# Kernel optimization log

Hardware: AMD Instinct MI355X
Metric: run time of the kernel (lower is better)

## Reference

```python
import jax, jax.numpy as jnp
import numpy as np

SHIFT_MIN, SHIFT_MAX = -14.0, 0.0  # deepshift range for weight_bits=5: (-(2**4-2), 0)


def shift_quant(w):
    """Quantize weights to signed powers of two (bit-shift weights), STE form."""
    sign = jnp.sign(w)
    shift = jnp.clip(jnp.round(jnp.log2(jnp.abs(w) + 1e-12)), SHIFT_MIN, SHIFT_MAX)
    q = sign * jnp.exp2(shift)
    return w + jax.lax.stop_gradient(q - w)


def moe_fc(t, wg, w0, b0, w1, b1):
    """Top-1 routing over 2 experts: expert0 dense Linear, expert1 shift-quantized Linear.
    t: [T, C]; weights torch-layout [out, in]. With top_k=1 the softmaxed top-k gate is 1.0,
    so combine is a hard select of the chosen expert's output."""
    logits = t @ wg                      # [T, 2]
    pick0 = (jnp.argmax(logits, axis=-1) == 0)[:, None]
    y0 = t @ w0.T + b0                   # dense expert
    y1 = t @ shift_quant(w1).T + b1      # shift expert
    return jnp.where(pick0, y0, y1)


def setup_inputs() -> dict:
    key = jax.random.key(0)
    ks = jax.random.split(key, 10)
    B, N, C, Dh = 16, 1024, 512, 2048
    s = 0.02
    return {
        "x": jax.random.normal(ks[0], (B, N, C), jnp.float32),
        "H": 32,
        "W": 32,
        "wg1": jax.random.normal(ks[1], (C, 2), jnp.float32) * s,
        "fc1_w0": jax.random.normal(ks[2], (Dh, C), jnp.float32) * s,
        "fc1_b0": jnp.zeros((Dh,), jnp.float32),
        "fc1_w1": jax.random.normal(ks[3], (Dh, C), jnp.float32) * s,
        "fc1_b1": jnp.zeros((Dh,), jnp.float32),
        "dw_w": jax.random.normal(ks[4], (Dh, 1, 3, 3), jnp.float32) * np.sqrt(2.0 / 9.0),
        "dw_b": jnp.zeros((Dh,), jnp.float32),
        "wg2": jax.random.normal(ks[5], (Dh, 2), jnp.float32) * s,
        "fc2_w0": jax.random.normal(ks[6], (C, Dh), jnp.float32) * s,
        "fc2_b0": jnp.zeros((C,), jnp.float32),
        "fc2_w1": jax.random.normal(ks[7], (C, Dh), jnp.float32) * s,
        "fc2_b1": jnp.zeros((C,), jnp.float32),
    }


def reference(x, H, W, wg1, fc1_w0, fc1_b0, fc1_w1, fc1_b1, dw_w, dw_b,
              wg2, fc2_w0, fc2_b0, fc2_w1, fc2_b1):
    B, N, C = x.shape
    Dh = fc1_w0.shape[0]
    # fc1 MoE
    h = moe_fc(x.reshape(-1, C), wg1, fc1_w0, fc1_b0, fc1_w1, fc1_b1)  # [B*N, Dh]
    # DWConv 3x3 depthwise, NCHW
    h = h.reshape(B, N, Dh).transpose(0, 2, 1).reshape(B, Dh, H, W)
    h = jax.lax.conv_general_dilated(
        h, dw_w, window_strides=(1, 1), padding="SAME",
        dimension_numbers=("NCHW", "OIHW", "NCHW"), feature_group_count=Dh)
    h = h + dw_b[None, :, None, None]
    h = h.reshape(B, Dh, N).transpose(0, 2, 1)  # [B, N, Dh]
    # GELU (exact, as nn.GELU default); dropout p=0 -> identity
    h = jax.nn.gelu(h, approximate=False)
    # fc2 MoE
    y = moe_fc(h.reshape(-1, Dh), wg2, fc2_w0, fc2_b0, fc2_w1, fc2_b1)
    return y.reshape(B, N, -1)
```

## Files before the change

### kernel.cpp

```cpp
#include <hip/hip_runtime.h>
#include <hip/hip_bf16.h>


#define TOKS  16384
#define CIN   512
#define DHID  2048

typedef __attribute__((ext_vector_type(8))) __bf16 bf16x8;
typedef __attribute__((ext_vector_type(4))) float  f32x4;
typedef __attribute__((ext_vector_type(4))) float  float4v;
typedef __attribute__((ext_vector_type(4))) unsigned short ushort4v;
typedef __attribute__((ext_vector_type(8))) unsigned short ushort8;

__device__ __forceinline__ unsigned short f2bf(float f) {
  union { float f; unsigned int u; } a; a.f = f;
  unsigned int u = a.u;
  unsigned int r = u + 0x7FFFu + ((u >> 16) & 1u);
  return (unsigned short)(r >> 16);
}
__device__ __forceinline__ float bf2f(unsigned short h) {
  union { unsigned int u; float f; } a; a.u = ((unsigned int)h) << 16;
  return a.f;
}

__device__ __forceinline__ float squant(float w) {
  if (w == 0.0f) return 0.0f;
  float aw = fabsf(w) + 1e-12f;
  union { float f; unsigned u; } a; a.f = aw;
  int e = (int)((a.u >> 23) & 0xFFu) - 127;
  unsigned frac = a.u & 0x7FFFFFu;
  int shift = e + (frac >= 0x3504F4u ? 1 : 0);
  shift = min(max(shift, -14), 0);
  union { unsigned u; float f; } q; q.u = (unsigned)(shift + 127) << 23;
  return (w > 0.0f) ? q.f : -q.f;
}

#define GLDS16(gp, lp) __builtin_amdgcn_global_load_lds(                      \
    (const __attribute__((address_space(1))) void*)(gp),                      \
    (__attribute__((address_space(3))) void*)(lp), 16, 0, 0)

#define SBAR()  { __builtin_amdgcn_s_barrier(); __builtin_amdgcn_sched_barrier(0); }
#define VMCNT(n) asm volatile("s_waitcnt vmcnt(" #n ")" ::: "memory")

__global__ void k_prep(const float* __restrict__ w0, const float* __restrict__ w1,
                       const float* __restrict__ w20, const float* __restrict__ w21,
                       unsigned short* __restrict__ w0hi, unsigned short* __restrict__ w0lo,
                       unsigned short* __restrict__ w1q, unsigned short* __restrict__ w20b,
                       unsigned short* __restrict__ w21b) {
  int i = blockIdx.x * 256 + threadIdx.x;
  if (i >= DHID * CIN) return;
  float v = w0[i];
  unsigned short h = f2bf(v);
  w0hi[i] = h;
  w0lo[i] = f2bf(v - bf2f(h));
  w1q[i]  = f2bf(squant(w1[i]));
  w20b[i] = f2bf(w20[i]);
  w21b[i] = f2bf(squant(w21[i]));
}

__global__ void k_prepg(const float* __restrict__ x, const float* __restrict__ wg1,
                        unsigned short* __restrict__ xhi, unsigned short* __restrict__ xlo,
                        unsigned char* __restrict__ pick1) {
  __shared__ float wg[1024];
  const int t = threadIdx.x;
  #pragma unroll
  for (int i = 0; i < 4; ++i) wg[t + i * 256] = wg1[t + i * 256];
  __syncthreads();
  const int tok = blockIdx.x * 4 + (t >> 6);
  const int l = t & 63;
  const float* xr = x + (size_t)tok * CIN + l * 8;
  float4v v0 = *(const float4v*)xr;
  float4v v1 = *(const float4v*)(xr + 4);
  float s0 = 0.f, s1 = 0.f;
  ushort8 hv, lv;
  #pragma unroll
  for (int j = 0; j < 8; ++j) {
    float v = (j < 4) ? v0[j] : v1[j - 4];
    unsigned short h = f2bf(v);
    hv[j] = h;
    lv[j] = f2bf(v - bf2f(h));
    int c = l * 8 + j;
    s0 += v * wg[c * 2];
    s1 += v * wg[c * 2 + 1];
  }
  *(ushort8*)&xhi[(size_t)tok * CIN + l * 8] = hv;
  *(ushort8*)&xlo[(size_t)tok * CIN + l * 8] = lv;
  for (int m = 32; m; m >>= 1) { s0 += __shfl_xor(s0, m); s1 += __shfl_xor(s1, m); }
  if (l == 0) pick1[tok] = (s0 >= s1) ? 0 : 1;
}

__global__ void k_scan(const unsigned char* __restrict__ pick, int* __restrict__ perm,
                       int* __restrict__ n0buf) {
  __shared__ int wpre[17];
  const int t = threadIdx.x;
  const int lane = t & 63, w = t >> 6;
  unsigned char loc[16]; int c0 = 0;
  #pragma unroll
  for (int i = 0; i < 16; ++i) { loc[i] = pick[t * 16 + i]; c0 += (loc[i] == 0); }
  int s = c0;
  #pragma unroll
  for (int off = 1; off < 64; off <<= 1) {
    int v = __shfl_up(s, off);
    if (lane >= off) s += v;
  }
  if (lane == 63) wpre[w + 1] = s;
  if (t == 0) wpre[0] = 0;
  __syncthreads();
  if (t == 0) {
    for (int j = 1; j <= 16; ++j) wpre[j] += wpre[j - 1];
    n0buf[0] = wpre[16];
  }
  __syncthreads();
  int total0 = wpre[16];
  int pre0 = wpre[w] + s - c0;
  int pre1 = t * 16 - pre0;
  int p0 = pre0, p1 = total0 + pre1;
  #pragma unroll
  for (int i = 0; i < 16; ++i) {
    int tok = t * 16 + i;
    if (loc[i] == 0) perm[p0++] = tok; else perm[p1++] = tok;
  }
}

__launch_bounds__(256, 2)
__global__ void k_fc1_e0(const unsigned short* __restrict__ xhi,
                         const unsigned short* __restrict__ xlo,
                         const unsigned short* __restrict__ w0hi,
                         const unsigned short* __restrict__ w0lo,
                         const float* __restrict__ b0,
                         const int* __restrict__ perm, const int* __restrict__ n0buf,
                         float* __restrict__ h32) {
  __shared__ unsigned short sm[24576];
  const int n0 = n0buf[0];
  const int t = threadIdx.x, wv = t >> 6, ln = t & 63;
  const int lr = ln & 15, lg = ln >> 4;
  const int g = blockIdx.x, q = g >> 3;
  const int tok0 = ((g & 7) + ((q >> 4) << 3)) * 128;
  const int nbase = (q & 15) * 128;
  if (tok0 >= n0) return;
  const int wm = (wv >> 1) * 64, wn = (wv & 1) * 64;

  int rowoff[4];
  #pragma unroll
  for (int mt = 0; mt < 4; ++mt)
    rowoff[mt] = perm[tok0 + wm + (mt << 4) + lr] * CIN + (lg << 3);

  const int swsrc = (((ln & 3) ^ ((ln >> 3) & 3)) << 3);
  const int swrd  = ((lg ^ ((lr >> 1) & 3)) << 3);

  f32x4 acc[4][4];
  #pragma unroll
  for (int i = 0; i < 4; ++i)
    #pragma unroll
    for (int j = 0; j < 4; ++j) acc[i][j] = f32x4{0.f, 0.f, 0.f, 0.f};

  auto STAGEB = [&](int kt, int db) {
    const int k0 = kt * 32;
    #pragma unroll
    for (int s = 0; s < 2; ++s) {
      const int rowblk = s * 4 + wv;
      size_t gb = (size_t)(nbase + (rowblk << 4) + (ln >> 2)) * CIN + k0 + swsrc;
      GLDS16(w0hi + gb, &sm[db * 8192 + (rowblk << 9)]);
      GLDS16(w0lo + gb, &sm[db * 8192 + 4096 + (rowblk << 9)]);
    }
  };
  auto LOADA = [&](bf16x8 (&ah)[4], bf16x8 (&al)[4], int kt) {
    const int k0 = kt * 32;
    #pragma unroll
    for (int mt = 0; mt < 4; ++mt) {
      ah[mt] = *(const bf16x8*)&xhi[rowoff[mt] + k0];
      al[mt] = *(const bf16x8*)&xlo[rowoff[mt] + k0];
    }
  };
  auto COMPUTE = [&](const bf16x8 (&ah)[4], const bf16x8 (&al)[4], int db) {
    __builtin_amdgcn_s_setprio(1);
    #pragma unroll
    for (int nt = 0; nt < 4; ++nt) {
      int bb = db * 8192 + (wn + (nt << 4) + lr) * 32 + swrd;
      bf16x8 bh = *(const bf16x8*)&sm[bb];
      bf16x8 bl = *(const bf16x8*)&sm[bb + 4096];
      #pragma unroll
      for (int mt = 0; mt < 4; ++mt) {
        acc[mt][nt] = __builtin_amdgcn_mfma_f32_16x16x32_bf16(ah[mt], bh, acc[mt][nt], 0, 0, 0);
        acc[mt][nt] = __builtin_amdgcn_mfma_f32_16x16x32_bf16(al[mt], bh, acc[mt][nt], 0, 0, 0);
        acc[mt][nt] = __builtin_amdgcn_mfma_f32_16x16x32_bf16(ah[mt], bl, acc[mt][nt], 0, 0, 0);
      }
    }
    __builtin_amdgcn_s_setprio(0);
  };

  bf16x8 Ah0[4], Al0[4], Ah1[4], Al1[4];
  LOADA(Ah0, Al0, 0);
  STAGEB(0, 0);
  STAGEB(1, 1);
  for (int kt = 0; kt < 14; kt += 2) {
    SBAR();
    LOADA(Ah1, Al1, kt + 1);
    STAGEB(kt + 2, (kt + 2) % 3);
    VMCNT(16);
    SBAR();
    COMPUTE(Ah0, Al0, kt % 3);
    SBAR();
    LOADA(Ah0, Al0, kt + 2);
    STAGEB(kt + 3, (kt + 3) % 3);
    VMCNT(16);
    SBAR();
    COMPUTE(Ah1, Al1, (kt + 1) % 3);
  }
  SBAR();
  LOADA(Ah1, Al1, 15);
  VMCNT(12);
  SBAR();
  COMPUTE(Ah0, Al0, 2);
  SBAR();
  VMCNT(0);
  SBAR();
  COMPUTE(Ah1, Al1, 0);

  __syncthreads();
  float* smf = (float*)sm;
  float bi[4];
  #pragma unroll
  for (int nt = 0; nt < 4; ++nt) bi[nt] = b0[nbase + wn + (nt << 4) + lr];
  #pragma unroll
  for (int mt = 0; mt < 4; ++mt) {
    #pragma unroll
    for (int nt = 0; nt < 4; ++nt) {
      f32x4 v = acc[mt][nt];
      #pragma unroll
      for (int rr = 0; rr < 4; ++rr)
        smf[wv * 1088 + ((lg << 2) + rr) * 68 + (nt << 4) + lr] = v[rr] + bi[nt];
    }
    #pragma unroll
    for (int p = 0; p < 4; ++p) {
      int row = (p << 2) + (ln >> 4);
      int pos = tok0 + wm + (mt << 4) + row;
      if (pos < n0) {
        f32x4 vv = *(const f32x4*)&smf[wv * 1088 + row * 68 + ((ln & 15) << 2)];
        *(f32x4*)&h32[(size_t)perm[pos] * DHID + nbase + wn + ((ln & 15) << 2)] = vv;
      }
    }
  }
}

__launch_bounds__(256, 2)
__global__ void k_fc1_e1(const unsigned short* __restrict__ xhi,
                         const unsigned short* __restrict__ xlo,
                         const unsigned short* __restrict__ w1q,
                         const float* __restrict__ b1,
                         const int* __restrict__ perm, const int* __restrict__ n0buf,
                         float* __restrict__ h32) {
  __shared__ unsigned short sm[12288];
  const int n0 = n0buf[0];
  const int t = threadIdx.x, wv = t >> 6, ln = t & 63;
  const int lr = ln & 15, lg = ln >> 4;
  const int g = blockIdx.x, q = g >> 3;
  const int tok0 = ((g & 7) + ((q >> 4) << 3)) * 128;
  const int nbase = (q & 15) * 128;
  if (tok0 + 128 <= n0) return;
  const int wm = (wv >> 1) * 64, wn = (wv & 1) * 64;

  int rowoff[4];
  #pragma unroll
  for (int mt = 0; mt < 4; ++mt)
    rowoff[mt] = perm[tok0 + wm + (mt << 4) + lr] * CIN + (lg << 3);

  const int swsrc = (((ln & 3) ^ ((ln >> 3) & 3)) << 3);
  const int swrd  = ((lg ^ ((lr >> 1) & 3)) << 3);

  f32x4 acc[4][4];
  #pragma unroll
  for (int i = 0; i < 4; ++i)
    #pragma unroll
    for (int j = 0; j < 4; ++j) acc[i][j] = f32x4{0.f, 0.f, 0.f, 0.f};

  auto STAGEB = [&](int kt, int db) {
    const int k0 = kt * 32;
    #pragma unroll
    for (int s = 0; s < 2; ++s) {
      const int rowblk = s * 4 + wv;
      size_t gb = (size_t)(nbase + (rowblk << 4) + (ln >> 2)) * CIN + k0 + swsrc;
      GLDS16(w1q + gb, &sm[db * 4096 + (rowblk << 9)]);
    }
  };
  auto LOADA = [&](bf16x8 (&ah)[4], bf16x8 (&al)[4], int kt) {
    const int k0 = kt * 32;
    #pragma unroll
    for (int mt = 0; mt < 4; ++mt) {
      ah[mt] = *(const bf16x8*)&xhi[rowoff[mt] + k0];
      al[mt] = *(const bf16x8*)&xlo[rowoff[mt] + k0];
    }
  };
  auto COMPUTE = [&](const bf16x8 (&ah)[4], const bf16x8 (&al)[4], int db) {
    __builtin_amdgcn_s_setprio(1);
    #pragma unroll
    for (int nt = 0; nt < 4; ++nt) {
      bf16x8 bq = *(const bf16x8*)&sm[db * 4096 + (wn + (nt << 4) + lr) * 32 + swrd];
      #pragma unroll
      for (int mt = 0; mt < 4; ++mt) {
        acc[mt][nt] = __builtin_amdgcn_mfma_f32_16x16x32_bf16(ah[mt], bq, acc[mt][nt], 0, 0, 0);
        acc[mt][nt] = __builtin_amdgcn_mfma_f32_16x16x32_bf16(al[mt], bq, acc[mt][nt], 0, 0, 0);
      }
    }
    __builtin_amdgcn_s_setprio(0);
  };

  bf16x8 Ah0[4], Al0[4], Ah1[4], Al1[4];
  LOADA(Ah0, Al0, 0);
  STAGEB(0, 0);
  STAGEB(1, 1);
  for (int kt = 0; kt < 14; kt += 2) {
    SBAR();
    LOADA(Ah1, Al1, kt + 1);
    STAGEB(kt + 2, (kt + 2) % 3);
    VMCNT(12);
    SBAR();
    COMPUTE(Ah0, Al0, kt % 3);
    SBAR();
    LOADA(Ah0, Al0, kt + 2);
    STAGEB(kt + 3, (kt + 3) % 3);
    VMCNT(12);
    SBAR();
    COMPUTE(Ah1, Al1, (kt + 1) % 3);
  }
  SBAR();
  LOADA(Ah1, Al1, 15);
  VMCNT(10);
  SBAR();
  COMPUTE(Ah0, Al0, 2);
  SBAR();
  VMCNT(0);
  SBAR();
  COMPUTE(Ah1, Al1, 0);

  __syncthreads();
  float* smf = (float*)sm;
  float bi[4];
  #pragma unroll
  for (int nt = 0; nt < 4; ++nt) bi[nt] = b1[nbase + wn + (nt << 4) + lr];
  #pragma unroll
  for (int mt = 0; mt < 4; ++mt) {
    #pragma unroll
    for (int nt = 0; nt < 4; ++nt) {
      f32x4 v = acc[mt][nt];
      #pragma unroll
      for (int rr = 0; rr < 4; ++rr)
        smf[wv * 1088 + ((lg << 2) + rr) * 68 + (nt << 4) + lr] = v[rr] + bi[nt];
    }
    #pragma unroll
    for (int p = 0; p < 4; ++p) {
      int row = (p << 2) + (ln >> 4);
      int pos = tok0 + wm + (mt << 4) + row;
      if (pos >= n0) {
        f32x4 vv = *(const f32x4*)&smf[wv * 1088 + row * 68 + ((ln & 15) << 2)];
        *(f32x4*)&h32[(size_t)perm[pos] * DHID + nbase + wn + ((ln & 15) << 2)] = vv;
      }
    }
  }
}

__launch_bounds__(256)
__global__ void k_conv(const float* __restrict__ h32, const float* __restrict__ dww,
                       const float* __restrict__ dwb, const float* __restrict__ wg2,
                       unsigned short* __restrict__ hb, float* __restrict__ part) {
  __shared__ float4v tile[10][32][8];
  const int dc = blockIdx.x;
  const int ys = blockIdx.y;
  const int b  = blockIdx.z;
  const int t = threadIdx.x;
  const int d0 = dc * 32, y0 = ys * 8;
  const int dl4 = t & 7, xq = t >> 3;

  #pragma unroll
  for (int ry = 0; ry < 10; ++ry) {
    int y = y0 - 1 + ry;
    float4v v = {0.f, 0.f, 0.f, 0.f};
    if (y >= 0 && y < 32)
      v = *(const float4v*)&h32[(size_t)(b * 1024 + y * 32 + xq) * DHID + d0 + dl4 * 4];
    tile[ry][xq][dl4] = v;
  }
  __syncthreads();

  const int d = d0 + dl4 * 4;
  float4v kk[9];
  #pragma unroll
  for (int i = 0; i < 9; ++i) {
    kk[i][0] = dww[(d + 0) * 9 + i]; kk[i][1] = dww[(d + 1) * 9 + i];
    kk[i][2] = dww[(d + 2) * 9 + i]; kk[i][3] = dww[(d + 3) * 9 + i];
  }
  const float4v bias = *(const float4v*)&dwb[d];
  float4v g0v, g1v;
  #pragma unroll
  for (int j = 0; j < 4; ++j) { g0v[j] = wg2[(d + j) * 2]; g1v[j] = wg2[(d + j) * 2 + 1]; }

  #pragma unroll
  for (int yy = 0; yy < 8; ++yy) {
    float4v s = bias;
    #pragma unroll
    for (int dy = 0; dy < 3; ++dy)
      #pragma unroll
      for (int dx = 0; dx < 3; ++dx) {
        int xs = xq + dx - 1;
        if (xs >= 0 && xs < 32) {
          float4v v = tile[yy + dy][xs][dl4];
          float4v k = kk[dy * 3 + dx];
          s[0] += v[0] * k[0]; s[1] += v[1] * k[1];
          s[2] += v[2] * k[2]; s[3] += v[3] * k[3];
        }
      }
    float4v gg;
    #pragma unroll
    for (int j = 0; j < 4; ++j)
      gg[j] = 0.5f * s[j] * (1.0f + erff(s[j] * 0.70710678118654752f));
    int tok = b * 1024 + (y0 + yy) * 32 + xq;
    ushort4v hv;
    #pragma unroll
    for (int j = 0; j < 4; ++j) hv[j] = f2bf(gg[j]);
    *(ushort4v*)&hb[(size_t)tok * DHID + d] = hv;
    float p0 = gg[0] * g0v[0] + gg[1] * g0v[1] + gg[2] * g0v[2] + gg[3] * g0v[3];
    float p1 = gg[0] * g1v[0] + gg[1] * g1v[1] + gg[2] * g1v[2] + gg[3] * g1v[3];
    p0 += __shfl_xor(p0, 1); p0 += __shfl_xor(p0, 2); p0 += __shfl_xor(p0, 4);
    p1 += __shfl_xor(p1, 1); p1 += __shfl_xor(p1, 2); p1 += __shfl_xor(p1, 4);
    if (dl4 == 0) {
      part[(size_t)tok * 128 + dc] = p0;
      part[(size_t)tok * 128 + 64 + dc] = p1;
    }
  }
}

__global__ void k_gate2(const float* __restrict__ part, unsigned char* __restrict__ pick2) {
  int tok = blockIdx.x * 4 + (threadIdx.x >> 6);
  int l = threadIdx.x & 63;
  const float* pr = part + (size_t)tok * 128;
  float s0 = pr[l], s1 = pr[64 + l];
  for (int m = 32; m; m >>= 1) { s0 += __shfl_xor(s0, m); s1 += __shfl_xor(s1, m); }
  if (l == 0) pick2[tok] = (s0 >= s1) ? 0 : 1;
}

template <int EXPERT>
__launch_bounds__(256, 2)
__global__ void k_fc2_e(const unsigned short* __restrict__ hb,
                        const unsigned short* __restrict__ wb,
                        const float* __restrict__ bias_v,
                        const int* __restrict__ perm, const int* __restrict__ n0buf,
                        float* __restrict__ out) {
  __shared__ unsigned short sm[24576];
  const int n0 = n0buf[0];
  const int t = threadIdx.x, wv = t >> 6, ln = t & 63;
  const int lr = ln & 15, lg = ln >> 4;
  const int g = blockIdx.x, q = g >> 3;
  const int tok0 = ((g & 7) + ((q >> 2) << 3)) * 128;
  const int nbase = (q & 3) * 128;
  if (EXPERT == 0) { if (tok0 >= n0) return; }
  else             { if (tok0 + 128 <= n0) return; }
  const int wm = (wv >> 1) * 64, wn = (wv & 1) * 64;

  int rowoff[4];
  #pragma unroll
  for (int mt = 0; mt < 4; ++mt)
    rowoff[mt] = perm[tok0 + wm + (mt << 4) + lr] * DHID + (lg << 3);

  const int swsrc = (((ln & 3) ^ ((ln >> 3) & 3)) << 3);
  const int swrd  = ((lg ^ ((lr >> 1) & 3)) << 3);

  f32x4 acc[4][4];
  #pragma unroll
  for (int i = 0; i < 4; ++i)
    #pragma unroll
    for (int j = 0; j < 4; ++j) acc[i][j] = f32x4{0.f, 0.f, 0.f, 0.f};

  auto STAGEB = [&](int kt, int db) {
    #pragma unroll
    for (int ks = 0; ks < 2; ++ks) {
      const int k0 = kt * 64 + ks * 32;
      #pragma unroll
      for (int s = 0; s < 2; ++s) {
        const int rowblk = s * 4 + wv;
        size_t gb = (size_t)(nbase + (rowblk << 4) + (ln >> 2)) * DHID + k0 + swsrc;
        GLDS16(wb + gb, &sm[db * 8192 + ks * 4096 + (rowblk << 9)]);
      }
    }
  };
  auto LOADA = [&](bf16x8 (&a)[8], int kt) {
    #pragma unroll
    for (int ks = 0; ks < 2; ++ks) {
      const int k0 = kt * 64 + ks * 32;
      #pragma unroll
      for (int mt = 0; mt < 4; ++mt)
        a[ks * 4 + mt] = *(const bf16x8*)&hb[rowoff[mt] + k0];
    }
  };
  auto COMPUTE = [&](const bf16x8 (&a)[8], int db) {
    __builtin_amdgcn_s_setprio(1);
    #pragma unroll
    for (int ks = 0; ks < 2; ++ks) {
      #pragma unroll
      for (int nt = 0; nt < 4; ++nt) {
        bf16x8 bf = *(const bf16x8*)&sm[db * 8192 + ks * 4096 + (wn + (nt << 4) + lr) * 32 + swrd];
        #pragma unroll
        for (int mt = 0; mt < 4; ++mt)
          acc[mt][nt] = __builtin_amdgcn_mfma_f32_16x16x32_bf16(a[ks * 4 + mt], bf, acc[mt][nt], 0, 0, 0);
      }
    }
    __builtin_amdgcn_s_setprio(0);
  };

  bf16x8 A0[8], A1[8];
  LOADA(A0, 0);
  STAGEB(0, 0);
  STAGEB(1, 1);
  for (int kt = 0; kt < 30; kt += 2) {
    SBAR();
    LOADA(A1, kt + 1);
    STAGEB(kt + 2, (kt + 2) % 3);
    VMCNT(16);
    SBAR();
    COMPUTE(A0, kt % 3);
    SBAR();
    LOADA(A0, kt + 2);
    STAGEB(kt + 3, (kt + 3) % 3);
    VMCNT(16);
    SBAR();
    COMPUTE(A1, (kt + 1) % 3);
  }
  SBAR();
  LOADA(A1, 31);
  VMCNT(12);
  SBAR();
  COMPUTE(A0, 0);
  SBAR();
  VMCNT(0);
  SBAR();
  COMPUTE(A1, 1);

  __syncthreads();
  float* smf = (float*)sm;
  float bi[4];
  #pragma unroll
  for (int nt = 0; nt < 4; ++nt) bi[nt] = bias_v[nbase + wn + (nt << 4) + lr];
  #pragma unroll
  for (int mt = 0; mt < 4; ++mt) {
    #pragma unroll
    for (int nt = 0; nt < 4; ++nt) {
      f32x4 v = acc[mt][nt];
      #pragma unroll
      for (int rr = 0; rr < 4; ++rr)
        smf[wv * 1088 + ((lg << 2) + rr) * 68 + (nt << 4) + lr] = v[rr] + bi[nt];
    }
    #pragma unroll
    for (int p = 0; p < 4; ++p) {
      int row = (p << 2) + (ln >> 4);
      int pos = tok0 + wm + (mt << 4) + row;
      bool store = (EXPERT == 0) ? (pos < n0) : (pos >= n0);
      if (store) {
        f32x4 vv = *(const f32x4*)&smf[wv * 1088 + row * 68 + ((ln & 15) << 2)];
        *(f32x4*)&out[(size_t)perm[pos] * CIN + nbase + wn + ((ln & 15) << 2)] = vv;
      }
    }
  }
}

extern "C" void kernel_launch(void* const* d_in, const int* in_sizes, int n_in,
                              void* d_out, int out_size, void* d_ws, size_t ws_size,
                              hipStream_t stream) {
  (void)in_sizes; (void)n_in; (void)out_size; (void)ws_size;
  const float* x   = (const float*)d_in[0];
  const float* wg1 = (const float*)d_in[3];
  const float* w0  = (const float*)d_in[4];
  const float* b0  = (const float*)d_in[5];
  const float* w1  = (const float*)d_in[6];
  const float* b1  = (const float*)d_in[7];
  const float* dww = (const float*)d_in[8];
  const float* dwb = (const float*)d_in[9];
  const float* wg2 = (const float*)d_in[10];
  const float* w20 = (const float*)d_in[11];
  const float* b20 = (const float*)d_in[12];
  const float* w21 = (const float*)d_in[13];
  const float* b21 = (const float*)d_in[14];
  float* out = (float*)d_out;

  char* ws = (char*)d_ws;
  const size_t MB2 = 1u << 21;
  unsigned short* w0hi = (unsigned short*)(ws + 0 * MB2);
  unsigned short* w0lo = (unsigned short*)(ws + 1 * MB2);
  unsigned short* w1q  = (unsigned short*)(ws + 2 * MB2);
  unsigned short* w20b = (unsigned short*)(ws + 3 * MB2);
  unsigned short* w21b = (unsigned short*)(ws + 4 * MB2);
  char* p = ws + 5 * MB2;
  unsigned short* xhi = (unsigned short*)p;            p += (size_t)TOKS * CIN * 2;
  unsigned short* xlo = (unsigned short*)p;            p += (size_t)TOKS * CIN * 2;
  unsigned char* pick1 = (unsigned char*)p;            p += 65536;
  unsigned char* pick2 = (unsigned char*)p;            p += 65536;
  int* perm1 = (int*)p;                                p += TOKS * 4;
  int* perm2 = (int*)p;                                p += TOKS * 4;
  int* n0a   = (int*)p;                                p += 256;
  int* n0b   = (int*)p;                                p += 256;
  float* part = (float*)p;                             p += (size_t)TOKS * 128 * 4;
  float* h32  = (float*)p;                             p += (size_t)TOKS * DHID * 4;
  unsigned short* hb = (unsigned short*)p;

  k_prep <<<4096, 256, 0, stream>>>(w0, w1, w20, w21, w0hi, w0lo, w1q, w20b, w21b);
  k_prepg<<<4096, 256, 0, stream>>>(x, wg1, xhi, xlo, pick1);
  k_scan <<<1, 1024, 0, stream>>>(pick1, perm1, n0a);
  k_fc1_e0<<<2048, 256, 0, stream>>>(xhi, xlo, w0hi, w0lo, b0, perm1, n0a, h32);
  k_fc1_e1<<<2048, 256, 0, stream>>>(xhi, xlo, w1q, b1, perm1, n0a, h32);
  k_conv <<<dim3(64, 4, 16), 256, 0, stream>>>(h32, dww, dwb, wg2, hb, part);
  k_gate2<<<4096, 256, 0, stream>>>(part, pick2);
  k_scan <<<1, 1024, 0, stream>>>(pick2, perm2, n0b);
  k_fc2_e<0><<<512, 256, 0, stream>>>(hb, w20b, b20, perm2, n0b, out);
  k_fc2_e<1><<<512, 256, 0, stream>>>(hb, w21b, b21, perm2, n0b, out);
}
```

Baseline: 418.0 us.

## Merge prep kernels, pipeline conv row strips via LDS, raise GEMM occupancy hints

Fuses the weight-prep and input-prep/gate kernels into one launch split by block index, which removes a kernel launch. The depthwise conv kernel now processes all four 8-row strips of a batch/channel chunk in one block. It double-buffers the strips in LDS using async global-to-LDS loads, with a zeroed scratch buffer standing in for out-of-range rows, so loads overlap compute and halo rows are no longer refetched. Launch bounds on the fc1/fc2 GEMMs are raised to request more waves per CU, which may force register spills.

```diff
diff --git a/kernel.cpp b/kernel.cpp
--- a/kernel.cpp
+++ b/kernel.cpp
@@ -46,27 +46,28 @@
                        const float* __restrict__ w20, const float* __restrict__ w21,
                        unsigned short* __restrict__ w0hi, unsigned short* __restrict__ w0lo,
                        unsigned short* __restrict__ w1q, unsigned short* __restrict__ w20b,
-                       unsigned short* __restrict__ w21b) {
-  int i = blockIdx.x * 256 + threadIdx.x;
-  if (i >= DHID * CIN) return;
-  float v = w0[i];
-  unsigned short h = f2bf(v);
-  w0hi[i] = h;
-  w0lo[i] = f2bf(v - bf2f(h));
-  w1q[i]  = f2bf(squant(w1[i]));
-  w20b[i] = f2bf(w20[i]);
-  w21b[i] = f2bf(squant(w21[i]));
-}
-
-__global__ void k_prepg(const float* __restrict__ x, const float* __restrict__ wg1,
-                        unsigned short* __restrict__ xhi, unsigned short* __restrict__ xlo,
-                        unsigned char* __restrict__ pick1) {
+                       unsigned short* __restrict__ w21b,
+                       const float* __restrict__ x, const float* __restrict__ wg1,
+                       unsigned short* __restrict__ xhi, unsigned short* __restrict__ xlo,
+                       unsigned char* __restrict__ pick1) {
   __shared__ float wg[1024];
   const int t = threadIdx.x;
+  if (blockIdx.x < 4096) {
+    int i = blockIdx.x * 256 + t;
+    float v = w0[i];
+    unsigned short h = f2bf(v);
+    w0hi[i] = h;
+    w0lo[i] = f2bf(v - bf2f(h));
+    w1q[i]  = f2bf(squant(w1[i]));
+    w20b[i] = f2bf(w20[i]);
+    w21b[i] = f2bf(squant(w21[i]));
+    return;
+  }
+  const int bid = blockIdx.x - 4096;
   #pragma unroll
   for (int i = 0; i < 4; ++i) wg[t + i * 256] = wg1[t + i * 256];
   __syncthreads();
-  const int tok = blockIdx.x * 4 + (t >> 6);
+  const int tok = bid * 4 + (t >> 6);
   const int l = t & 63;
   const float* xr = x + (size_t)tok * CIN + l * 8;
   float4v v0 = *(const float4v*)xr;
@@ -122,7 +123,7 @@
   }
 }
 
-__launch_bounds__(256, 2)
+__launch_bounds__(256, 3)
 __global__ void k_fc1_e0(const unsigned short* __restrict__ xhi,
                          const unsigned short* __restrict__ xlo,
                          const unsigned short* __restrict__ w0hi,
@@ -243,7 +244,7 @@
   }
 }
 
-__launch_bounds__(256, 2)
+__launch_bounds__(256, 4)
 __global__ void k_fc1_e1(const unsigned short* __restrict__ xhi,
                          const unsigned short* __restrict__ xlo,
                          const unsigned short* __restrict__ w1q,
@@ -359,27 +360,32 @@
   }
 }
 
-__launch_bounds__(256)
-__global__ void k_conv(const float* __restrict__ h32, const float* __restrict__ dww,
-                       const float* __restrict__ dwb, const float* __restrict__ wg2,
+__launch_bounds__(256, 2)
+__global__ void k_conv(const float* __restrict__ h32, const float* __restrict__ zbuf,
+                       const float* __restrict__ dww, const float* __restrict__ dwb,
+                       const float* __restrict__ wg2,
                        unsigned short* __restrict__ hb, float* __restrict__ part) {
-  __shared__ float4v tile[10][32][8];
-  const int dc = blockIdx.x;
-  const int ys = blockIdx.y;
-  const int b  = blockIdx.z;
-  const int t = threadIdx.x;
-  const int d0 = dc * 32, y0 = ys * 8;
+  __shared__ float4v tile[2][10][32][8];
+  const int dc = blockIdx.x & 63;
+  const int b  = blockIdx.x >> 6;
+  const int t = threadIdx.x, wv = t >> 6, ln = t & 63;
+  const int d0 = dc * 32;
   const int dl4 = t & 7, xq = t >> 3;
 
-  #pragma unroll
-  for (int ry = 0; ry < 10; ++ry) {
-    int y = y0 - 1 + ry;
-    float4v v = {0.f, 0.f, 0.f, 0.f};
-    if (y >= 0 && y < 32)
-      v = *(const float4v*)&h32[(size_t)(b * 1024 + y * 32 + xq) * DHID + d0 + dl4 * 4];
-    tile[ry][xq][dl4] = v;
-  }
-  __syncthreads();
+  auto STAGE = [&](int s, int db) {
+    const int y0 = s * 8;
+    #pragma unroll
+    for (int i = 0; i < 10; ++i) {
+      int gi = wv * 10 + i;
+      int ry = gi >> 2, qq = gi & 3;
+      int y = y0 - 1 + ry;
+      int sxq = qq * 8 + (ln >> 3);
+      const float* src = (y >= 0 && y < 32)
+        ? &h32[(size_t)((b << 10) + y * 32 + sxq) * DHID + d0 + (ln & 7) * 4]
+        : &zbuf[ln * 4];
+      GLDS16(src, &tile[db][ry][qq * 8][0]);
+    }
+  };
 
   const int d = d0 + dl4 * 4;
   float4v kk[9];
@@ -393,38 +399,50 @@
   #pragma unroll
   for (int j = 0; j < 4; ++j) { g0v[j] = wg2[(d + j) * 2]; g1v[j] = wg2[(d + j) * 2 + 1]; }
 
-  #pragma unroll
-  for (int yy = 0; yy < 8; ++yy) {
-    float4v s = bias;
-    #pragma unroll
-    for (int dy = 0; dy < 3; ++dy)
-      #pragma unroll
-      for (int dx = 0; dx < 3; ++dx) {
-        int xs = xq + dx - 1;
-        if (xs >= 0 && xs < 32) {
-          float4v v = tile[yy + dy][xs][dl4];
-          float4v k = kk[dy * 3 + dx];
-          s[0] += v[0] * k[0]; s[1] += v[1] * k[1];
-          s[2] += v[2] * k[2]; s[3] += v[3] * k[3];
+  STAGE(0, 0);
+  for (int s = 0; s < 4; ++s) {
+    if (s < 3) {
+      STAGE(s + 1, (s + 1) & 1);
+      VMCNT(10);
+    } else {
+      VMCNT(0);
+    }
+    SBAR();
+    const int db = s & 1, y0 = s * 8;
+    #pragma unroll
+    for (int yy = 0; yy < 8; ++yy) {
+      float4v sum = bias;
+      #pragma unroll
+      for (int dy = 0; dy < 3; ++dy)
+        #pragma unroll
+        for (int dx = 0; dx < 3; ++dx) {
+          int xs = xq + dx - 1;
+          if (xs >= 0 && xs < 32) {
+            float4v v = tile[db][yy + dy][xs][dl4];
+            float4v k = kk[dy * 3 + dx];
+            sum[0] += v[0] * k[0]; sum[1] += v[1] * k[1];
+            sum[2] += v[2] * k[2]; sum[3] += v[3] * k[3];
+          }
         }
-      }
-    float4v gg;
-    #pragma unroll
-    for (int j = 0; j < 4; ++j)
-      gg[j] = 0.5f * s[j] * (1.0f + erff(s[j] * 0.70710678118654752f));
-    int tok = b * 1024 + (y0 + yy) * 32 + xq;
-    ushort4v hv;
-    #pragma unroll
-    for (int j = 0; j < 4; ++j) hv[j] = f2bf(gg[j]);
-    *(ushort4v*)&hb[(size_t)tok * DHID + d] = hv;
-    float p0 = gg[0] * g0v[0] + gg[1] * g0v[1] + gg[2] * g0v[2] + gg[3] * g0v[3];
-    float p1 = gg[0] * g1v[0] + gg[1] * g1v[1] + gg[2] * g1v[2] + gg[3] * g1v[3];
-    p0 += __shfl_xor(p0, 1); p0 += __shfl_xor(p0, 2); p0 += __shfl_xor(p0, 4);
-    p1 += __shfl_xor(p1, 1); p1 += __shfl_xor(p1, 2); p1 += __shfl_xor(p1, 4);
-    if (dl4 == 0) {
-      part[(size_t)tok * 128 + dc] = p0;
-      part[(size_t)tok * 128 + 64 + dc] = p1;
-    }
+      float4v gg;
+      #pragma unroll
+      for (int j = 0; j < 4; ++j)
+        gg[j] = 0.5f * sum[j] * (1.0f + erff(sum[j] * 0.70710678118654752f));
+      int tok = (b << 10) + (y0 + yy) * 32 + xq;
+      ushort4v hv;
+      #pragma unroll
+      for (int j = 0; j < 4; ++j) hv[j] = f2bf(gg[j]);
+      *(ushort4v*)&hb[(size_t)tok * DHID + d] = hv;
+      float p0 = gg[0] * g0v[0] + gg[1] * g0v[1] + gg[2] * g0v[2] + gg[3] * g0v[3];
+      float p1 = gg[0] * g1v[0] + gg[1] * g1v[1] + gg[2] * g1v[2] + gg[3] * g1v[3];
+      p0 += __shfl_xor(p0, 1); p0 += __shfl_xor(p0, 2); p0 += __shfl_xor(p0, 4);
+      p1 += __shfl_xor(p1, 1); p1 += __shfl_xor(p1, 2); p1 += __shfl_xor(p1, 4);
+      if (dl4 == 0) {
+        part[(size_t)tok * 128 + dc] = p0;
+        part[(size_t)tok * 128 + 64 + dc] = p1;
+      }
+    }
+    SBAR();
   }
 }
 
@@ -438,7 +456,7 @@
 }
 
 template <int EXPERT>
-__launch_bounds__(256, 2)
+__launch_bounds__(256, 3)
 __global__ void k_fc2_e(const unsigned short* __restrict__ hb,
                         const unsigned short* __restrict__ wb,
                         const float* __restrict__ bias_v,
@@ -595,16 +613,18 @@
   int* perm2 = (int*)p;                                p += TOKS * 4;
   int* n0a   = (int*)p;                                p += 256;
   int* n0b   = (int*)p;                                p += 256;
+  float* zbuf = (float*)p;                             p += 4096;
   float* part = (float*)p;                             p += (size_t)TOKS * 128 * 4;
   float* h32  = (float*)p;                             p += (size_t)TOKS * DHID * 4;
   unsigned short* hb = (unsigned short*)p;
 
-  k_prep <<<4096, 256, 0, stream>>>(w0, w1, w20, w21, w0hi, w0lo, w1q, w20b, w21b);
-  k_prepg<<<4096, 256, 0, stream>>>(x, wg1, xhi, xlo, pick1);
+  hipMemsetAsync(zbuf, 0, 4096, stream);
+  k_prep <<<8192, 256, 0, stream>>>(w0, w1, w20, w21, w0hi, w0lo, w1q, w20b, w21b,
+                                    x, wg1, xhi, xlo, pick1);
   k_scan <<<1, 1024, 0, stream>>>(pick1, perm1, n0a);
   k_fc1_e0<<<2048, 256, 0, stream>>>(xhi, xlo, w0hi, w0lo, b0, perm1, n0a, h32);
   k_fc1_e1<<<2048, 256, 0, stream>>>(xhi, xlo, w1q, b1, perm1, n0a, h32);
-  k_conv <<<dim3(64, 4, 16), 256, 0, stream>>>(h32, dww, dwb, wg2, hb, part);
+  k_conv <<<1024, 256, 0, stream>>>(h32, zbuf, dww, dwb, wg2, hb, part);
   k_gate2<<<4096, 256, 0, stream>>>(part, pick2);
   k_scan <<<1, 1024, 0, stream>>>(pick2, perm2, n0b);
   k_fc2_e<0><<<512, 256, 0, stream>>>(hb, w20b, b20, perm2, n0b, out);
```

Result: slower. 690.9 us (+65.3%).

## Merge prep kernels, use fast erf GELU, transpose gate partial sums

Applied to the files above, without the earlier changes.

Combines the weight-prep and input-prep kernels into one launch that branches on block index. Replaces the library erff in the conv GELU with an Abramowitz-Stegun polynomial that uses hardware exp2 and reciprocal. Stores the gate-2 partial sums in a token-major transposed layout so k_gate2 can run one thread per token with coalesced loads instead of a wave-level shuffle reduction. This saves a launch and some transcendental cost, but the polynomial erf (error around 1e-7 absolute) may flip borderline routing decisions and shift results slightly.

```diff
diff --git a/kernel.cpp b/kernel.cpp
--- a/kernel.cpp
+++ b/kernel.cpp
@@ -35,6 +35,30 @@
   return (w > 0.0f) ? q.f : -q.f;
 }
 
+__device__ __forceinline__ float gelu_fast(float s) {
+  float z = fabsf(s) * 0.70710678118654752f;
+  float zz = z * z;
+#if __has_builtin(__builtin_amdgcn_exp2f)
+  float e = __builtin_amdgcn_exp2f(zz * -1.4426950408889634f);
+#else
+  float e = exp2f(zz * -1.4426950408889634f);
+#endif
+  float d = fmaf(0.3275911f, z, 1.0f);
+#if __has_builtin(__builtin_amdgcn_rcpf)
+  float t = __builtin_amdgcn_rcpf(d);
+#else
+  float t = 1.0f / d;
+#endif
+  float p = fmaf(1.061405429f, t, -1.453152027f);
+  p = fmaf(p, t, 1.421413741f);
+  p = fmaf(p, t, -0.284496736f);
+  p = fmaf(p, t, 0.254829592f);
+  p = p * t;
+  float erfz = fmaf(-p, e, 1.0f);
+  float er = (s < 0.0f) ? -erfz : erfz;
+  return 0.5f * s * (1.0f + er);
+}
+
 #define GLDS16(gp, lp) __builtin_amdgcn_global_load_lds(                      \
     (const __attribute__((address_space(1))) void*)(gp),                      \
     (__attribute__((address_space(3))) void*)(lp), 16, 0, 0)
@@ -46,27 +70,28 @@
                        const float* __restrict__ w20, const float* __restrict__ w21,
                        unsigned short* __restrict__ w0hi, unsigned short* __restrict__ w0lo,
                        unsigned short* __restrict__ w1q, unsigned short* __restrict__ w20b,
-                       unsigned short* __restrict__ w21b) {
-  int i = blockIdx.x * 256 + threadIdx.x;
-  if (i >= DHID * CIN) return;
-  float v = w0[i];
-  unsigned short h = f2bf(v);
-  w0hi[i] = h;
-  w0lo[i] = f2bf(v - bf2f(h));
-  w1q[i]  = f2bf(squant(w1[i]));
-  w20b[i] = f2bf(w20[i]);
-  w21b[i] = f2bf(squant(w21[i]));
-}
-
-__global__ void k_prepg(const float* __restrict__ x, const float* __restrict__ wg1,
-                        unsigned short* __restrict__ xhi, unsigned short* __restrict__ xlo,
-                        unsigned char* __restrict__ pick1) {
+                       unsigned short* __restrict__ w21b,
+                       const float* __restrict__ x, const float* __restrict__ wg1,
+                       unsigned short* __restrict__ xhi, unsigned short* __restrict__ xlo,
+                       unsigned char* __restrict__ pick1) {
   __shared__ float wg[1024];
   const int t = threadIdx.x;
+  if (blockIdx.x < 4096) {
+    int i = blockIdx.x * 256 + t;
+    float v = w0[i];
+    unsigned short h = f2bf(v);
+    w0hi[i] = h;
+    w0lo[i] = f2bf(v - bf2f(h));
+    w1q[i]  = f2bf(squant(w1[i]));
+    w20b[i] = f2bf(w20[i]);
+    w21b[i] = f2bf(squant(w21[i]));
+    return;
+  }
+  const int bid = blockIdx.x - 4096;
   #pragma unroll
   for (int i = 0; i < 4; ++i) wg[t + i * 256] = wg1[t + i * 256];
   __syncthreads();
-  const int tok = blockIdx.x * 4 + (t >> 6);
+  const int tok = bid * 4 + (t >> 6);
   const int l = t & 63;
   const float* xr = x + (size_t)tok * CIN + l * 8;
   float4v v0 = *(const float4v*)xr;
@@ -410,8 +435,7 @@
       }
     float4v gg;
     #pragma unroll
-    for (int j = 0; j < 4; ++j)
-      gg[j] = 0.5f * s[j] * (1.0f + erff(s[j] * 0.70710678118654752f));
+    for (int j = 0; j < 4; ++j) gg[j] = gelu_fast(s[j]);
     int tok = b * 1024 + (y0 + yy) * 32 + xq;
     ushort4v hv;
     #pragma unroll
@@ -422,19 +446,20 @@
     p0 += __shfl_xor(p0, 1); p0 += __shfl_xor(p0, 2); p0 += __shfl_xor(p0, 4);
     p1 += __shfl_xor(p1, 1); p1 += __shfl_xor(p1, 2); p1 += __shfl_xor(p1, 4);
     if (dl4 == 0) {
-      part[(size_t)tok * 128 + dc] = p0;
-      part[(size_t)tok * 128 + 64 + dc] = p1;
+      part[(size_t)dc * TOKS + tok] = p0;
+      part[(size_t)(64 + dc) * TOKS + tok] = p1;
     }
   }
 }
 
 __global__ void k_gate2(const float* __restrict__ part, unsigned char* __restrict__ pick2) {
-  int tok = blockIdx.x * 4 + (threadIdx.x >> 6);
-  int l = threadIdx.x & 63;
-  const float* pr = part + (size_t)tok * 128;
-  float s0 = pr[l], s1 = pr[64 + l];
-  for (int m = 32; m; m >>= 1) { s0 += __shfl_xor(s0, m); s1 += __shfl_xor(s1, m); }
-  if (l == 0) pick2[tok] = (s0 >= s1) ? 0 : 1;
+  int tok = blockIdx.x * 256 + threadIdx.x;
+  float s0 = 0.f, s1 = 0.f;
+  for (int i = 0; i < 64; ++i) {
+    s0 += part[(size_t)i * TOKS + tok];
+    s1 += part[(size_t)(64 + i) * TOKS + tok];
+  }
+  pick2[tok] = (s0 >= s1) ? 0 : 1;
 }
 
 template <int EXPERT>
@@ -599,13 +624,13 @@
   float* h32  = (float*)p;                             p += (size_t)TOKS * DHID * 4;
   unsigned short* hb = (unsigned short*)p;
 
-  k_prep <<<4096, 256, 0, stream>>>(w0, w1, w20, w21, w0hi, w0lo, w1q, w20b, w21b);
-  k_prepg<<<4096, 256, 0, stream>>>(x, wg1, xhi, xlo, pick1);
+  k_prep <<<8192, 256, 0, stream>>>(w0, w1, w20, w21, w0hi, w0lo, w1q, w20b, w21b,
+                                    x, wg1, xhi, xlo, pick1);
   k_scan <<<1, 1024, 0, stream>>>(pick1, perm1, n0a);
   k_fc1_e0<<<2048, 256, 0, stream>>>(xhi, xlo, w0hi, w0lo, b0, perm1, n0a, h32);
   k_fc1_e1<<<2048, 256, 0, stream>>>(xhi, xlo, w1q, b1, perm1, n0a, h32);
   k_conv <<<dim3(64, 4, 16), 256, 0, stream>>>(h32, dww, dwb, wg2, hb, part);
-  k_gate2<<<4096, 256, 0, stream>>>(part, pick2);
+  k_gate2<<<64, 256, 0, stream>>>(part, pick2);
   k_scan <<<1, 1024, 0, stream>>>(pick2, perm2, n0b);
   k_fc2_e<0><<<512, 256, 0, stream>>>(hb, w20b, b20, perm2, n0b, out);
   k_fc2_e<1><<<512, 256, 0, stream>>>(hb, w21b, b21, perm2, n0b, out);
```

New measurement: 401.8 us. 1.04x faster.
